# Optimization experiments

Measured on AMD Instinct MI355X. Metric: run time of the kernel, lower is better.

## Reference

```python
import jax, jax.numpy as jnp
import numpy as np
import math

B, S, H, D = 4, 2048, 16, 64
HID = H * D  # 1024


def setup_inputs() -> dict:
    key = jax.random.key(0)
    ks = jax.random.split(key, 9)
    s_in = 1.0 / math.sqrt(D)
    s_hid = 1.0 / math.sqrt(HID)
    return {
        "x": jax.random.normal(ks[0], (B, S, D), dtype=jnp.float32),
        "Wq": jax.random.uniform(ks[1], (D, HID), jnp.float32, -s_in, s_in),
        "bq": jax.random.uniform(ks[2], (HID,), jnp.float32, -s_in, s_in),
        "Wk": jax.random.uniform(ks[3], (D, HID), jnp.float32, -s_in, s_in),
        "bk": jax.random.uniform(ks[4], (HID,), jnp.float32, -s_in, s_in),
        "Wv": jax.random.uniform(ks[5], (D, HID), jnp.float32, -s_in, s_in),
        "bv": jax.random.uniform(ks[6], (HID,), jnp.float32, -s_in, s_in),
        "Wo": jax.random.uniform(ks[7], (HID, D), jnp.float32, -s_hid, s_hid),
        "bo": jax.random.uniform(ks[8], (D,), jnp.float32, -s_hid, s_hid),
    }


def reference(x, Wq, bq, Wk, bk, Wv, bv, Wo, bo):
    b, s, _ = x.shape
    # projections: [B,S,D] -> [B,S,HID] -> [B,H,S,D]
    q = (x @ Wq + bq).reshape(b, s, H, D).transpose(0, 2, 1, 3)
    k = (x @ Wk + bk).reshape(b, s, H, D).transpose(0, 2, 1, 3)
    v = (x @ Wv + bv).reshape(b, s, H, D).transpose(0, 2, 1, 3)
    scores = jnp.einsum("bhqd,bhkd->bhqk", q, k) / math.sqrt(D)
    # causal mask: -inf strictly above the diagonal
    causal = jnp.tril(jnp.ones((s, s), dtype=bool))
    scores = jnp.where(causal, scores, -jnp.inf)
    attn = jax.nn.softmax(scores, axis=-1)  # dropout is identity at eval
    out = jnp.einsum("bhqk,bhkd->bhqd", attn, v)
    out = out.transpose(0, 2, 1, 3).reshape(b, s, HID)
    return out @ Wo + bo  # [B,S,D]
```

## Files before the change

### kernel.cpp

```cpp
#include <hip/hip_runtime.h>
#include <hip/hip_bf16.h>

#define B 4
#define S 2048
#define H 16
#define D 64
#define HID 1024

typedef __hip_bfloat16 bf16;
typedef __attribute__((ext_vector_type(8))) short bf16x8;
typedef __attribute__((ext_vector_type(4))) short bf16x4;
typedef __attribute__((ext_vector_type(4))) float f32x4;

static __device__ __forceinline__ float b2f(bf16 v) { return __bfloat162float(v); }

static __device__ __forceinline__ unsigned pkbf(float a, float b) {
    union { bf16 h; unsigned short u; } ua, ub;
    ua.h = __float2bfloat16(a);
    ub.h = __float2bfloat16(b);
    return (unsigned)ua.u | ((unsigned)ub.u << 16);
}

#define SCL 0.18033688011112042f

#define QSTR 72
#define VTS  136

__global__ __launch_bounds__(256) void qkv_mfma_kernel(
    const float* __restrict__ x,
    const float* __restrict__ Wq, const float* __restrict__ bq,
    const float* __restrict__ Wk, const float* __restrict__ bk,
    const float* __restrict__ Wv, const float* __restrict__ bv,
    bf16* __restrict__ q, bf16* __restrict__ k, bf16* __restrict__ v)
{
    __shared__ __align__(16) char smem[36864];
    __shared__ float bs[128];
    bf16* Xs = (bf16*)smem;
    bf16* Wt = (bf16*)(smem + 128 * QSTR * 2);

    const int tid = threadIdx.x;
    const int mat = blockIdx.y >> 3;
    const int N0  = (blockIdx.y & 7) * 128;
    const int m0  = blockIdx.x * 128;

    const float* W    = (mat == 0) ? Wq : (mat == 1) ? Wk : Wv;
    const float* bias = (mat == 0) ? bq : (mat == 1) ? bk : bv;
    bf16*        dst  = (mat == 0) ? q  : (mat == 1) ? k  : v;
    const float  oscale = (mat == 0) ? SCL : 1.0f;

    #pragma unroll
    for (int i = 0; i < 8; ++i) {
        int item = i * 256 + tid;
        int row = item >> 4, f4 = item & 15;
        float4 xv = *(const float4*)&x[(size_t)(m0 + row) * D + f4 * 4];
        union { bf16 h[4]; bf16x4 v4; } u;
        u.h[0] = __float2bfloat16(xv.x); u.h[1] = __float2bfloat16(xv.y);
        u.h[2] = __float2bfloat16(xv.z); u.h[3] = __float2bfloat16(xv.w);
        *(bf16x4*)&Xs[row * QSTR + f4 * 4] = u.v4;
    }
    #pragma unroll
    for (int i = 0; i < 2; ++i) {
        int unit = i * 256 + tid;
        int n0 = (unit & 31) * 4, k0 = (unit >> 5) * 4;
        float wv[4][4];
        #pragma unroll
        for (int j = 0; j < 4; ++j) {
            float4 t = *(const float4*)&W[(size_t)(k0 + j) * HID + N0 + n0];
            wv[j][0] = t.x; wv[j][1] = t.y; wv[j][2] = t.z; wv[j][3] = t.w;
        }
        #pragma unroll
        for (int dn = 0; dn < 4; ++dn) {
            union { bf16 h[4]; bf16x4 v4; } u;
            #pragma unroll
            for (int j = 0; j < 4; ++j) u.h[j] = __float2bfloat16(wv[j][dn]);
            *(bf16x4*)&Wt[(n0 + dn) * QSTR + k0] = u.v4;
        }
    }
    if (tid < 128) bs[tid] = bias[N0 + tid];
    __syncthreads();

    const int lane = tid & 63, wave = tid >> 6;
    const int c = lane & 15, quad = lane >> 4;

    bf16x8 af[2][2];
    #pragma unroll
    for (int mg = 0; mg < 2; ++mg)
        #pragma unroll
        for (int kc = 0; kc < 2; ++kc)
            af[mg][kc] = *(const bf16x8*)&Xs[(wave * 32 + mg * 16 + c) * QSTR + kc * 32 + quad * 8];

    f32x4 acc[2][8];
    #pragma unroll
    for (int mg = 0; mg < 2; ++mg)
        #pragma unroll
        for (int ng = 0; ng < 8; ++ng)
            acc[mg][ng] = (f32x4){0.f, 0.f, 0.f, 0.f};

    #pragma unroll
    for (int ng = 0; ng < 8; ++ng) {
        bf16x8 bf0 = *(const bf16x8*)&Wt[(ng * 16 + c) * QSTR + quad * 8];
        bf16x8 bf1 = *(const bf16x8*)&Wt[(ng * 16 + c) * QSTR + 32 + quad * 8];
        #pragma unroll
        for (int mg = 0; mg < 2; ++mg) {
            acc[mg][ng] = __builtin_amdgcn_mfma_f32_16x16x32_bf16(af[mg][0], bf0, acc[mg][ng], 0, 0, 0);
            acc[mg][ng] = __builtin_amdgcn_mfma_f32_16x16x32_bf16(af[mg][1], bf1, acc[mg][ng], 0, 0, 0);
        }
    }

    if (mat == 2) {
        bf16* T = (bf16*)smem;
        __syncthreads();
        #pragma unroll
        for (int ng = 0; ng < 8; ++ng) {
            int hid_l = ng * 16 + c;
            float bb_ = bs[hid_l];
            #pragma unroll
            for (int mg = 0; mg < 2; ++mg) {
                int ss_l = wave * 32 + mg * 16 + quad * 4;
                union { bf16 h4[4]; bf16x4 v4; } u;
                #pragma unroll
                for (int r = 0; r < 4; ++r)
                    u.h4[r] = __float2bfloat16(acc[mg][ng][r] + bb_);
                *(bf16x4*)&T[hid_l * VTS + ss_l] = u.v4;
            }
        }
        __syncthreads();
        const int b_ = m0 >> 11, ss0 = m0 & (S - 1);
        #pragma unroll
        for (int pass = 0; pass < 8; ++pass) {
            int unit = pass * 256 + tid;
            int dd_l = unit >> 4, u8 = unit & 15;
            bf16x8 val = *(const bf16x8*)&T[dd_l * VTS + u8 * 8];
            int h = (N0 >> 6) + (dd_l >> 6), ddg = dd_l & 63;
            *(bf16x8*)&dst[((size_t)(b_ * H + h) * D + ddg) * S + ss0 + u8 * 8] = val;
        }
    } else {
        #pragma unroll
        for (int ng = 0; ng < 8; ++ng) {
            int n_g = N0 + ng * 16 + c;
            int h = n_g >> 6, dd = n_g & 63;
            float bb_ = bs[ng * 16 + c];
            #pragma unroll
            for (int mg = 0; mg < 2; ++mg) {
                #pragma unroll
                for (int r = 0; r < 4; ++r) {
                    int row = m0 + wave * 32 + mg * 16 + quad * 4 + r;
                    int b_ = row >> 11, ss = row & (S - 1);
                    dst[((size_t)(b_ * H + h) * S + ss) * D + dd] =
                        __float2bfloat16((acc[mg][ng][r] + bb_) * oscale);
                }
            }
        }
    }
}

#define BT   64
#define NT   (S / BT)
#define KSTR 72
#define PST  72

__global__ __launch_bounds__(256) void flash_mfma_kernel(
    const bf16* __restrict__ qg, const bf16* __restrict__ kg,
    const bf16* __restrict__ vg, bf16* __restrict__ og)
{
    __shared__ bf16 Ks[BT * KSTR];
    __shared__ bf16 Vt[BT * KSTR];
    __shared__ bf16 PsB[4][16 * PST];
    __shared__ bf16 PsA[4][16 * PST];

    const int tid  = threadIdx.x;
    const int wave = tid >> 6;
    const int lane = tid & 63;
    const int c    = lane & 15;
    const int quad = lane >> 4;

    const int L    = (int)blockIdx.x + 16 * (int)blockIdx.y;
    const int xcd  = L & 7;
    const int slot = L >> 3;
    const int pair = slot & 15;
    const int bh   = xcd * 8 + (slot >> 4);
    const int b_   = bh >> 4, h_ = bh & 15;
    const size_t hbase = (size_t)bh * S * D;
    bf16* myPB = &PsB[wave][0];
    bf16* myPA = &PsA[wave][0];
    const int srow = wave * 16 + c;

    const int qta = pair;
    const int qtb = NT - 1 - pair;

    const int sr0 = tid >> 3,         sc0 = (tid & 7) * 8;
    const int sr1 = (tid + 256) >> 3, sc1 = sc0;

    bf16x8 qfa0, qfa1, qfb0, qfb1;
    {
        const size_t ra = hbase + (size_t)(qta * BT + srow) * D;
        const size_t rb = hbase + (size_t)(qtb * BT + srow) * D;
        qfa0 = *(const bf16x8*)(qg + ra + quad * 8);
        qfa1 = *(const bf16x8*)(qg + ra + 32 + quad * 8);
        qfb0 = *(const bf16x8*)(qg + rb + quad * 8);
        qfb1 = *(const bf16x8*)(qg + rb + 32 + quad * 8);
    }

    bf16x8 kreg0, kreg1, vreg0, vreg1;
    kreg0 = *(const bf16x8*)(kg + hbase + (size_t)sr0 * D + sc0);
    kreg1 = *(const bf16x8*)(kg + hbase + (size_t)sr1 * D + sc1);
    vreg0 = *(const bf16x8*)(vg + hbase + (size_t)sr0 * S + sc0);
    vreg1 = *(const bf16x8*)(vg + hbase + (size_t)sr1 * S + sc1);

    float la = 0.f, lb = 0.f;
    f32x4 ota[4], otb[4];
    #pragma unroll
    for (int jn = 0; jn < 4; ++jn) {
        ota[jn] = (f32x4){0.f, 0.f, 0.f, 0.f};
        otb[jn] = (f32x4){0.f, 0.f, 0.f, 0.f};
    }

    auto front = [&](bf16x8 qf0, bf16x8 qf1, bf16* Pdst, float& l1, bool diag) {
        f32x4 st[4];
        #pragma unroll
        for (int jn = 0; jn < 4; ++jn) {
            bf16x8 kf0 = *(const bf16x8*)&Ks[(jn * 16 + c) * KSTR + quad * 8];
            bf16x8 kf1 = *(const bf16x8*)&Ks[(jn * 16 + c) * KSTR + 32 + quad * 8];
            f32x4 s = {0.f, 0.f, 0.f, 0.f};
            s = __builtin_amdgcn_mfma_f32_16x16x32_bf16(kf0, qf0, s, 0, 0, 0);
            s = __builtin_amdgcn_mfma_f32_16x16x32_bf16(kf1, qf1, s, 0, 0, 0);
            st[jn] = s;
        }
        #pragma unroll
        for (int jn = 0; jn < 4; ++jn) {
            float p0 = __builtin_amdgcn_exp2f(st[jn][0]);
            float p1 = __builtin_amdgcn_exp2f(st[jn][1]);
            float p2 = __builtin_amdgcn_exp2f(st[jn][2]);
            float p3 = __builtin_amdgcn_exp2f(st[jn][3]);
            if (diag) {
                int col = jn * 16 + quad * 4;
                if (col     > srow) p0 = 0.f;
                if (col + 1 > srow) p1 = 0.f;
                if (col + 2 > srow) p2 = 0.f;
                if (col + 3 > srow) p3 = 0.f;
            }
            l1 += (p0 + p1) + (p2 + p3);
            uint2 pk;
            pk.x = pkbf(p0, p1);
            pk.y = pkbf(p2, p3);
            *(uint2*)&Pdst[c * PST + jn * 16 + quad * 4] = pk;
        }
    };
    auto pv = [&](const bf16* Psrc, f32x4* ot) {
        #pragma unroll
        for (int kc = 0; kc < 2; ++kc) {
            bf16x8 pf = *(const bf16x8*)&Psrc[c * PST + kc * 32 + quad * 8];
            #pragma unroll
            for (int jn = 0; jn < 4; ++jn) {
                bf16x8 vf = *(const bf16x8*)&Vt[(jn * 16 + c) * KSTR + kc * 32 + quad * 8];
                ot[jn] = __builtin_amdgcn_mfma_f32_16x16x32_bf16(vf, pf, ot[jn], 0, 0, 0);
            }
        }
    };

    for (int kt = 0; kt <= qtb; ++kt) {
        __syncthreads();
        *(bf16x8*)&Ks[sr0 * KSTR + sc0] = kreg0;
        *(bf16x8*)&Ks[sr1 * KSTR + sc1] = kreg1;
        *(bf16x8*)&Vt[sr0 * KSTR + sc0] = vreg0;
        *(bf16x8*)&Vt[sr1 * KSTR + sc1] = vreg1;
        __syncthreads();

        if (kt < qtb) {
            const int nb = (kt + 1) * BT;
            kreg0 = *(const bf16x8*)(kg + hbase + (size_t)(nb + sr0) * D + sc0);
            kreg1 = *(const bf16x8*)(kg + hbase + (size_t)(nb + sr1) * D + sc1);
            vreg0 = *(const bf16x8*)(vg + hbase + (size_t)sr0 * S + nb + sc0);
            vreg1 = *(const bf16x8*)(vg + hbase + (size_t)sr1 * S + nb + sc1);
        }

        const bool withA = (kt <= qta);
        front(qfb0, qfb1, myPB, lb, kt == qtb);
        if (withA) front(qfa0, qfa1, myPA, la, kt == qta);
        asm volatile("s_waitcnt lgkmcnt(0)" ::: "memory");
        pv(myPB, otb);
        if (withA) pv(myPA, ota);
    }

    {
        float lt = lb;
        lt += __shfl_xor(lt, 16);
        lt += __shfl_xor(lt, 32);
        const float inv = 1.f / lt;
        const size_t obase = ((size_t)(b_ * S + qtb * BT + srow)) * HID + h_ * 64 + quad * 4;
        #pragma unroll
        for (int jn = 0; jn < 4; ++jn) {
            union { bf16 h4[4]; bf16x4 v4; } u;
            #pragma unroll
            for (int r = 0; r < 4; ++r)
                u.h4[r] = __float2bfloat16(otb[jn][r] * inv);
            *(bf16x4*)&og[obase + jn * 16] = u.v4;
        }
    }
    {
        float lt = la;
        lt += __shfl_xor(lt, 16);
        lt += __shfl_xor(lt, 32);
        const float inv = 1.f / lt;
        const size_t obase = ((size_t)(b_ * S + qta * BT + srow)) * HID + h_ * 64 + quad * 4;
        #pragma unroll
        for (int jn = 0; jn < 4; ++jn) {
            union { bf16 h4[4]; bf16x4 v4; } u;
            #pragma unroll
            for (int r = 0; r < 4; ++r)
                u.h4[r] = __float2bfloat16(ota[jn][r] * inv);
            *(bf16x4*)&og[obase + jn * 16] = u.v4;
        }
    }
}

__global__ __launch_bounds__(256) void out_proj_mfma_kernel(
    const bf16* __restrict__ o, const float* __restrict__ Wo,
    const float* __restrict__ bo, float* __restrict__ out)
{
    __shared__ bf16 Os[32 * QSTR];
    __shared__ bf16 Wot[64 * QSTR];
    __shared__ float bos[64];

    const int tid = threadIdx.x;
    const int m0  = blockIdx.x * 32;
    const int lane = tid & 63, wave = tid >> 6;
    const int c = lane & 15, quad = lane >> 4;
    const int mtile = wave >> 1;
    const int ngb   = (wave & 1) * 2;

    if (tid < 64) bos[tid] = bo[tid];

    f32x4 acc[2];
    acc[0] = (f32x4){0.f, 0.f, 0.f, 0.f};
    acc[1] = (f32x4){0.f, 0.f, 0.f, 0.f};

    for (int chunk = 0; chunk < 16; ++chunk) {
        const int k0 = chunk * 64;
        __syncthreads();
        {
            int row = tid >> 3, oct = tid & 7;
            *(bf16x8*)&Os[row * QSTR + oct * 8] =
                *(const bf16x8*)(o + (size_t)(m0 + row) * HID + k0 + oct * 8);
        }
        {
            int n0 = (tid & 15) * 4, kk0 = (tid >> 4) * 4;
            float wv[4][4];
            #pragma unroll
            for (int j = 0; j < 4; ++j) {
                float4 t = *(const float4*)&Wo[(size_t)(k0 + kk0 + j) * 64 + n0];
                wv[j][0] = t.x; wv[j][1] = t.y; wv[j][2] = t.z; wv[j][3] = t.w;
            }
            #pragma unroll
            for (int dn = 0; dn < 4; ++dn) {
                union { bf16 h[4]; bf16x4 v4; } u;
                #pragma unroll
                for (int j = 0; j < 4; ++j) u.h[j] = __float2bfloat16(wv[j][dn]);
                *(bf16x4*)&Wot[(n0 + dn) * QSTR + kk0] = u.v4;
            }
        }
        __syncthreads();

        bf16x8 a0 = *(const bf16x8*)&Os[(mtile * 16 + c) * QSTR + quad * 8];
        bf16x8 a1 = *(const bf16x8*)&Os[(mtile * 16 + c) * QSTR + 32 + quad * 8];
        #pragma unroll
        for (int g = 0; g < 2; ++g) {
            int ng = ngb + g;
            bf16x8 b0 = *(const bf16x8*)&Wot[(ng * 16 + c) * QSTR + quad * 8];
            bf16x8 b1 = *(const bf16x8*)&Wot[(ng * 16 + c) * QSTR + 32 + quad * 8];
            acc[g] = __builtin_amdgcn_mfma_f32_16x16x32_bf16(a0, b0, acc[g], 0, 0, 0);
            acc[g] = __builtin_amdgcn_mfma_f32_16x16x32_bf16(a1, b1, acc[g], 0, 0, 0);
        }
    }

    #pragma unroll
    for (int g = 0; g < 2; ++g) {
        int n = (ngb + g) * 16 + c;
        float bb_ = bos[n];
        #pragma unroll
        for (int r = 0; r < 4; ++r) {
            int row = m0 + mtile * 16 + quad * 4 + r;
            out[(size_t)row * 64 + n] = acc[g][r] + bb_;
        }
    }
}

extern "C" void kernel_launch(void* const* d_in, const int* in_sizes, int n_in,
                              void* d_out, int out_size, void* d_ws, size_t ws_size,
                              hipStream_t stream)
{
    const float* x  = (const float*)d_in[0];
    const float* Wq = (const float*)d_in[1];
    const float* bq = (const float*)d_in[2];
    const float* Wk = (const float*)d_in[3];
    const float* bk = (const float*)d_in[4];
    const float* Wv = (const float*)d_in[5];
    const float* bv = (const float*)d_in[6];
    const float* Wo = (const float*)d_in[7];
    const float* bo = (const float*)d_in[8];

    char* ws = (char*)d_ws;
    const size_t qkv_bytes = (size_t)B * S * HID * sizeof(bf16);
    bf16* qw = (bf16*)(ws);
    bf16* kw = (bf16*)(ws + qkv_bytes);
    bf16* vw = (bf16*)(ws + 2 * qkv_bytes);
    bf16* ow = (bf16*)(ws + 3 * qkv_bytes);

    qkv_mfma_kernel<<<dim3(B * S / 128, 24), 256, 0, stream>>>(
        x, Wq, bq, Wk, bk, Wv, bv, qw, kw, vw);

    flash_mfma_kernel<<<dim3(NT / 2, B * H), 256, 0, stream>>>(qw, kw, vw, ow);

    out_proj_mfma_kernel<<<dim3(B * S / 32), 256, 0, stream>>>(ow, Wo, bo,
                                                               (float*)d_out);
}
```

Before: 172.4 us.

## Load K/V fragments directly from global in flash kernel; prefetch out-proj tiles

The flash attention kernel no longer stages K and V tiles through shared memory with two block barriers per iteration. Each wave now loads its MFMA K and V fragments straight from global memory (via L1/L2), and the A and B query tiles are interleaved to share those fragments. This removes LDS traffic and __syncthreads, but every wave redundantly fetches the whole K/V tile and the loads are no longer prefetched a tile ahead, so global latency may be exposed. The output projection kernel also gains register double-buffering, issuing the next chunk's O and Wo loads after the barrier so they overlap the MFMAs.

```diff
diff --git a/kernel.cpp b/kernel.cpp
--- a/kernel.cpp
+++ b/kernel.cpp
@@ -156,15 +156,12 @@
 
 #define BT   64
 #define NT   (S / BT)
-#define KSTR 72
 #define PST  72
 
 __global__ __launch_bounds__(256) void flash_mfma_kernel(
     const bf16* __restrict__ qg, const bf16* __restrict__ kg,
     const bf16* __restrict__ vg, bf16* __restrict__ og)
 {
-    __shared__ bf16 Ks[BT * KSTR];
-    __shared__ bf16 Vt[BT * KSTR];
     __shared__ bf16 PsB[4][16 * PST];
     __shared__ bf16 PsA[4][16 * PST];
 
@@ -188,9 +185,6 @@
     const int qta = pair;
     const int qtb = NT - 1 - pair;
 
-    const int sr0 = tid >> 3,         sc0 = (tid & 7) * 8;
-    const int sr1 = (tid + 256) >> 3, sc1 = sc0;
-
     bf16x8 qfa0, qfa1, qfb0, qfb1;
     {
         const size_t ra = hbase + (size_t)(qta * BT + srow) * D;
@@ -201,11 +195,8 @@
         qfb1 = *(const bf16x8*)(qg + rb + 32 + quad * 8);
     }
 
-    bf16x8 kreg0, kreg1, vreg0, vreg1;
-    kreg0 = *(const bf16x8*)(kg + hbase + (size_t)sr0 * D + sc0);
-    kreg1 = *(const bf16x8*)(kg + hbase + (size_t)sr1 * D + sc1);
-    vreg0 = *(const bf16x8*)(vg + hbase + (size_t)sr0 * S + sc0);
-    vreg1 = *(const bf16x8*)(vg + hbase + (size_t)sr1 * S + sc1);
+    const bf16* kbase = kg + hbase + (size_t)c * D + quad * 8;
+    const bf16* vbase = vg + hbase + (size_t)c * S + quad * 8;
 
     float la = 0.f, lb = 0.f;
     f32x4 ota[4], otb[4];
@@ -215,71 +206,99 @@
         otb[jn] = (f32x4){0.f, 0.f, 0.f, 0.f};
     }
 
-    auto front = [&](bf16x8 qf0, bf16x8 qf1, bf16* Pdst, float& l1, bool diag) {
-        f32x4 st[4];
+    for (int kt = 0; kt <= qtb; ++kt) {
+        const bool withA = (kt <= qta);
+
+        bf16x8 kf[4][2];
+        {
+            const bf16* kp = kbase + (size_t)(kt * BT) * D;
+            #pragma unroll
+            for (int jn = 0; jn < 4; ++jn) {
+                kf[jn][0] = *(const bf16x8*)(kp + (size_t)(jn * 16) * D);
+                kf[jn][1] = *(const bf16x8*)(kp + (size_t)(jn * 16) * D + 32);
+            }
+        }
+
+        f32x4 stB[4], stA[4];
         #pragma unroll
         for (int jn = 0; jn < 4; ++jn) {
-            bf16x8 kf0 = *(const bf16x8*)&Ks[(jn * 16 + c) * KSTR + quad * 8];
-            bf16x8 kf1 = *(const bf16x8*)&Ks[(jn * 16 + c) * KSTR + 32 + quad * 8];
             f32x4 s = {0.f, 0.f, 0.f, 0.f};
-            s = __builtin_amdgcn_mfma_f32_16x16x32_bf16(kf0, qf0, s, 0, 0, 0);
-            s = __builtin_amdgcn_mfma_f32_16x16x32_bf16(kf1, qf1, s, 0, 0, 0);
-            st[jn] = s;
-        }
+            s = __builtin_amdgcn_mfma_f32_16x16x32_bf16(kf[jn][0], qfb0, s, 0, 0, 0);
+            s = __builtin_amdgcn_mfma_f32_16x16x32_bf16(kf[jn][1], qfb1, s, 0, 0, 0);
+            stB[jn] = s;
+            if (withA) {
+                f32x4 t = {0.f, 0.f, 0.f, 0.f};
+                t = __builtin_amdgcn_mfma_f32_16x16x32_bf16(kf[jn][0], qfa0, t, 0, 0, 0);
+                t = __builtin_amdgcn_mfma_f32_16x16x32_bf16(kf[jn][1], qfa1, t, 0, 0, 0);
+                stA[jn] = t;
+            }
+        }
+
+        bf16x8 vf[4][2];
+        {
+            const bf16* vp = vbase + kt * BT;
+            #pragma unroll
+            for (int jn = 0; jn < 4; ++jn) {
+                vf[jn][0] = *(const bf16x8*)(vp + (size_t)(jn * 16) * S);
+                vf[jn][1] = *(const bf16x8*)(vp + (size_t)(jn * 16) * S + 32);
+            }
+        }
+
         #pragma unroll
         for (int jn = 0; jn < 4; ++jn) {
-            float p0 = __builtin_amdgcn_exp2f(st[jn][0]);
-            float p1 = __builtin_amdgcn_exp2f(st[jn][1]);
-            float p2 = __builtin_amdgcn_exp2f(st[jn][2]);
-            float p3 = __builtin_amdgcn_exp2f(st[jn][3]);
-            if (diag) {
+            float p0 = __builtin_amdgcn_exp2f(stB[jn][0]);
+            float p1 = __builtin_amdgcn_exp2f(stB[jn][1]);
+            float p2 = __builtin_amdgcn_exp2f(stB[jn][2]);
+            float p3 = __builtin_amdgcn_exp2f(stB[jn][3]);
+            if (kt == qtb) {
                 int col = jn * 16 + quad * 4;
                 if (col     > srow) p0 = 0.f;
                 if (col + 1 > srow) p1 = 0.f;
                 if (col + 2 > srow) p2 = 0.f;
                 if (col + 3 > srow) p3 = 0.f;
             }
-            l1 += (p0 + p1) + (p2 + p3);
+            lb += (p0 + p1) + (p2 + p3);
             uint2 pk;
             pk.x = pkbf(p0, p1);
             pk.y = pkbf(p2, p3);
-            *(uint2*)&Pdst[c * PST + jn * 16 + quad * 4] = pk;
-        }
-    };
-    auto pv = [&](const bf16* Psrc, f32x4* ot) {
+            *(uint2*)&myPB[c * PST + jn * 16 + quad * 4] = pk;
+        }
+        if (withA) {
+            #pragma unroll
+            for (int jn = 0; jn < 4; ++jn) {
+                float p0 = __builtin_amdgcn_exp2f(stA[jn][0]);
+                float p1 = __builtin_amdgcn_exp2f(stA[jn][1]);
+                float p2 = __builtin_amdgcn_exp2f(stA[jn][2]);
+                float p3 = __builtin_amdgcn_exp2f(stA[jn][3]);
+                if (kt == qta) {
+                    int col = jn * 16 + quad * 4;
+                    if (col     > srow) p0 = 0.f;
+                    if (col + 1 > srow) p1 = 0.f;
+                    if (col + 2 > srow) p2 = 0.f;
+                    if (col + 3 > srow) p3 = 0.f;
+                }
+                la += (p0 + p1) + (p2 + p3);
+                uint2 pk;
+                pk.x = pkbf(p0, p1);
+                pk.y = pkbf(p2, p3);
+                *(uint2*)&myPA[c * PST + jn * 16 + quad * 4] = pk;
+            }
+        }
+
+        asm volatile("s_waitcnt lgkmcnt(0)" ::: "memory");
+
         #pragma unroll
         for (int kc = 0; kc < 2; ++kc) {
-            bf16x8 pf = *(const bf16x8*)&Psrc[c * PST + kc * 32 + quad * 8];
+            bf16x8 pfB = *(const bf16x8*)&myPB[c * PST + kc * 32 + quad * 8];
+            bf16x8 pfA;
+            if (withA) pfA = *(const bf16x8*)&myPA[c * PST + kc * 32 + quad * 8];
             #pragma unroll
             for (int jn = 0; jn < 4; ++jn) {
-                bf16x8 vf = *(const bf16x8*)&Vt[(jn * 16 + c) * KSTR + kc * 32 + quad * 8];
-                ot[jn] = __builtin_amdgcn_mfma_f32_16x16x32_bf16(vf, pf, ot[jn], 0, 0, 0);
-            }
-        }
-    };
-
-    for (int kt = 0; kt <= qtb; ++kt) {
-        __syncthreads();
-        *(bf16x8*)&Ks[sr0 * KSTR + sc0] = kreg0;
-        *(bf16x8*)&Ks[sr1 * KSTR + sc1] = kreg1;
-        *(bf16x8*)&Vt[sr0 * KSTR + sc0] = vreg0;
-        *(bf16x8*)&Vt[sr1 * KSTR + sc1] = vreg1;
-        __syncthreads();
-
-        if (kt < qtb) {
-            const int nb = (kt + 1) * BT;
-            kreg0 = *(const bf16x8*)(kg + hbase + (size_t)(nb + sr0) * D + sc0);
-            kreg1 = *(const bf16x8*)(kg + hbase + (size_t)(nb + sr1) * D + sc1);
-            vreg0 = *(const bf16x8*)(vg + hbase + (size_t)sr0 * S + nb + sc0);
-            vreg1 = *(const bf16x8*)(vg + hbase + (size_t)sr1 * S + nb + sc1);
-        }
-
-        const bool withA = (kt <= qta);
-        front(qfb0, qfb1, myPB, lb, kt == qtb);
-        if (withA) front(qfa0, qfa1, myPA, la, kt == qta);
-        asm volatile("s_waitcnt lgkmcnt(0)" ::: "memory");
-        pv(myPB, otb);
-        if (withA) pv(myPA, ota);
+                otb[jn] = __builtin_amdgcn_mfma_f32_16x16x32_bf16(vf[jn][kc], pfB, otb[jn], 0, 0, 0);
+                if (withA)
+                    ota[jn] = __builtin_amdgcn_mfma_f32_16x16x32_bf16(vf[jn][kc], pfA, ota[jn], 0, 0, 0);
+            }
+        }
     }
 
     {
@@ -329,37 +348,42 @@
     const int mtile = wave >> 1;
     const int ngb   = (wave & 1) * 2;
 
+    const int orow = tid >> 3, ooct = tid & 7;
+    const int n0 = (tid & 15) * 4, kk0 = (tid >> 4) * 4;
+
     if (tid < 64) bos[tid] = bo[tid];
+
+    bf16x8 oreg = *(const bf16x8*)(o + (size_t)(m0 + orow) * HID + ooct * 8);
+    float4 w4[4];
+    #pragma unroll
+    for (int j = 0; j < 4; ++j)
+        w4[j] = *(const float4*)&Wo[(size_t)(kk0 + j) * 64 + n0];
 
     f32x4 acc[2];
     acc[0] = (f32x4){0.f, 0.f, 0.f, 0.f};
     acc[1] = (f32x4){0.f, 0.f, 0.f, 0.f};
 
     for (int chunk = 0; chunk < 16; ++chunk) {
-        const int k0 = chunk * 64;
         __syncthreads();
-        {
-            int row = tid >> 3, oct = tid & 7;
-            *(bf16x8*)&Os[row * QSTR + oct * 8] =
-                *(const bf16x8*)(o + (size_t)(m0 + row) * HID + k0 + oct * 8);
-        }
-        {
-            int n0 = (tid & 15) * 4, kk0 = (tid >> 4) * 4;
-            float wv[4][4];
-            #pragma unroll
-            for (int j = 0; j < 4; ++j) {
-                float4 t = *(const float4*)&Wo[(size_t)(k0 + kk0 + j) * 64 + n0];
-                wv[j][0] = t.x; wv[j][1] = t.y; wv[j][2] = t.z; wv[j][3] = t.w;
-            }
-            #pragma unroll
-            for (int dn = 0; dn < 4; ++dn) {
-                union { bf16 h[4]; bf16x4 v4; } u;
-                #pragma unroll
-                for (int j = 0; j < 4; ++j) u.h[j] = __float2bfloat16(wv[j][dn]);
-                *(bf16x4*)&Wot[(n0 + dn) * QSTR + kk0] = u.v4;
-            }
+        *(bf16x8*)&Os[orow * QSTR + ooct * 8] = oreg;
+        #pragma unroll
+        for (int dn = 0; dn < 4; ++dn) {
+            union { bf16 h[4]; bf16x4 v4; } u;
+            u.h[0] = __float2bfloat16((&w4[0].x)[dn]);
+            u.h[1] = __float2bfloat16((&w4[1].x)[dn]);
+            u.h[2] = __float2bfloat16((&w4[2].x)[dn]);
+            u.h[3] = __float2bfloat16((&w4[3].x)[dn]);
+            *(bf16x4*)&Wot[(n0 + dn) * QSTR + kk0] = u.v4;
         }
         __syncthreads();
+
+        if (chunk < 15) {
+            const int k1 = (chunk + 1) * 64;
+            oreg = *(const bf16x8*)(o + (size_t)(m0 + orow) * HID + k1 + ooct * 8);
+            #pragma unroll
+            for (int j = 0; j < 4; ++j)
+                w4[j] = *(const float4*)&Wo[(size_t)(k1 + kk0 + j) * 64 + n0];
+        }
 
         bf16x8 a0 = *(const bf16x8*)&Os[(mtile * 16 + c) * QSTR + quad * 8];
         bf16x8 a1 = *(const bf16x8*)&Os[(mtile * 16 + c) * QSTR + 32 + quad * 8];
```

Result: slower. 313.8 us (+81.9%).

## Stage Q/K projection stores through LDS and prefetch out-proj tiles into registers

Applied to the files above, without the earlier changes.

In the QKV kernel, the non-transposed Q/K outputs are now written to a shared-memory tile first. They are then stored to global memory as 16-byte vectors instead of scattered 2-byte writes. The transpose tile stride changes from 136 to 132. The output projection kernel now loads the next chunk of O and Wo into registers while the current chunk computes, so global latency overlaps with MFMA work. This costs extra LDS syncs and register pressure, and the new stride may change bank conflicts and row alignment for the 16-byte stores.

```diff
diff --git a/kernel.cpp b/kernel.cpp
--- a/kernel.cpp
+++ b/kernel.cpp
@@ -24,7 +24,7 @@
 #define SCL 0.18033688011112042f
 
 #define QSTR 72
-#define VTS  136
+#define VTS  132
 
 __global__ __launch_bounds__(256) void qkv_mfma_kernel(
     const float* __restrict__ x,
@@ -135,21 +135,31 @@
             *(bf16x8*)&dst[((size_t)(b_ * H + h) * D + ddg) * S + ss0 + u8 * 8] = val;
         }
     } else {
+        bf16* T2 = (bf16*)smem;
+        __syncthreads();
         #pragma unroll
         for (int ng = 0; ng < 8; ++ng) {
-            int n_g = N0 + ng * 16 + c;
+            int n_l = ng * 16 + c;
+            float bb_ = bs[n_l];
+            #pragma unroll
+            for (int mg = 0; mg < 2; ++mg) {
+                int row0 = wave * 32 + mg * 16 + quad * 4;
+                #pragma unroll
+                for (int r = 0; r < 4; ++r)
+                    T2[(row0 + r) * VTS + n_l] =
+                        __float2bfloat16((acc[mg][ng][r] + bb_) * oscale);
+            }
+        }
+        __syncthreads();
+        const int b_ = m0 >> 11, ss0 = m0 & (S - 1);
+        #pragma unroll
+        for (int pass = 0; pass < 8; ++pass) {
+            int unit = pass * 256 + tid;
+            int row_l = unit >> 4, n8 = unit & 15;
+            bf16x8 val = *(const bf16x8*)&T2[row_l * VTS + n8 * 8];
+            int n_g = N0 + n8 * 8;
             int h = n_g >> 6, dd = n_g & 63;
-            float bb_ = bs[ng * 16 + c];
-            #pragma unroll
-            for (int mg = 0; mg < 2; ++mg) {
-                #pragma unroll
-                for (int r = 0; r < 4; ++r) {
-                    int row = m0 + wave * 32 + mg * 16 + quad * 4 + r;
-                    int b_ = row >> 11, ss = row & (S - 1);
-                    dst[((size_t)(b_ * H + h) * S + ss) * D + dd] =
-                        __float2bfloat16((acc[mg][ng][r] + bb_) * oscale);
-                }
-            }
+            *(bf16x8*)&dst[((size_t)(b_ * H + h) * S + ss0 + row_l) * D + dd] = val;
         }
     }
 }
@@ -329,37 +339,42 @@
     const int mtile = wave >> 1;
     const int ngb   = (wave & 1) * 2;
 
+    const int orow = tid >> 3, ooct = tid & 7;
+    const int n0 = (tid & 15) * 4, kk0 = (tid >> 4) * 4;
+
     if (tid < 64) bos[tid] = bo[tid];
+
+    bf16x8 oreg = *(const bf16x8*)(o + (size_t)(m0 + orow) * HID + ooct * 8);
+    float4 w4[4];
+    #pragma unroll
+    for (int j = 0; j < 4; ++j)
+        w4[j] = *(const float4*)&Wo[(size_t)(kk0 + j) * 64 + n0];
 
     f32x4 acc[2];
     acc[0] = (f32x4){0.f, 0.f, 0.f, 0.f};
     acc[1] = (f32x4){0.f, 0.f, 0.f, 0.f};
 
     for (int chunk = 0; chunk < 16; ++chunk) {
-        const int k0 = chunk * 64;
-        __syncthreads();
-        {
-            int row = tid >> 3, oct = tid & 7;
-            *(bf16x8*)&Os[row * QSTR + oct * 8] =
-                *(const bf16x8*)(o + (size_t)(m0 + row) * HID + k0 + oct * 8);
-        }
-        {
-            int n0 = (tid & 15) * 4, kk0 = (tid >> 4) * 4;
-            float wv[4][4];
-            #pragma unroll
-            for (int j = 0; j < 4; ++j) {
-                float4 t = *(const float4*)&Wo[(size_t)(k0 + kk0 + j) * 64 + n0];
-                wv[j][0] = t.x; wv[j][1] = t.y; wv[j][2] = t.z; wv[j][3] = t.w;
-            }
-            #pragma unroll
-            for (int dn = 0; dn < 4; ++dn) {
-                union { bf16 h[4]; bf16x4 v4; } u;
-                #pragma unroll
-                for (int j = 0; j < 4; ++j) u.h[j] = __float2bfloat16(wv[j][dn]);
-                *(bf16x4*)&Wot[(n0 + dn) * QSTR + kk0] = u.v4;
-            }
-        }
-        __syncthreads();
+        __syncthreads();
+        *(bf16x8*)&Os[orow * QSTR + ooct * 8] = oreg;
+        #pragma unroll
+        for (int dn = 0; dn < 4; ++dn) {
+            union { bf16 h[4]; bf16x4 v4; } u;
+            u.h[0] = __float2bfloat16((&w4[0].x)[dn]);
+            u.h[1] = __float2bfloat16((&w4[1].x)[dn]);
+            u.h[2] = __float2bfloat16((&w4[2].x)[dn]);
+            u.h[3] = __float2bfloat16((&w4[3].x)[dn]);
+            *(bf16x4*)&Wot[(n0 + dn) * QSTR + kk0] = u.v4;
+        }
+        __syncthreads();
+
+        if (chunk < 15) {
+            const int k1 = (chunk + 1) * 64;
+            oreg = *(const bf16x8*)(o + (size_t)(m0 + orow) * HID + k1 + ooct * 8);
+            #pragma unroll
+            for (int j = 0; j < 4; ++j)
+                w4[j] = *(const float4*)&Wo[(size_t)(k1 + kk0 + j) * 64 + n0];
+        }
 
         bf16x8 a0 = *(const bf16x8*)&Os[(mtile * 16 + c) * QSTR + quad * 8];
         bf16x8 a1 = *(const bf16x8*)&Os[(mtile * 16 + c) * QSTR + 32 + quad * 8];
```

After: 172.7 us, median of 2. No clear change (+0.2%).
